# Kernel optimization log

Measured on AMD Instinct MI355X. Metric: run time of the kernel, lower is better.

## Reference

```python
import jax, jax.numpy as jnp
import numpy as np

N = 50000      # nodes
E = 500000     # edges (includes N self-loops)
DIN = 512
DOUT = 256
NEG_SLOPE = 0.01  # torch nn.LeakyReLU default


def setup_inputs() -> dict:
    key = jax.random.key(0)
    k1, k2, k3, k4, k5 = jax.random.split(key, 5)
    x = jax.random.normal(k1, (N, DIN), dtype=jnp.float32)
    # xavier_normal_ with gain=1.414
    std_W = 1.414 * np.sqrt(2.0 / (DIN + DOUT))
    W = jax.random.normal(k2, (DIN, DOUT), dtype=jnp.float32) * std_W
    std_a = 1.414 * np.sqrt(2.0 / (1 + 2 * DOUT))
    a = jax.random.normal(k3, (2 * DOUT,), dtype=jnp.float32) * std_a
    # first N edges are self-loops so every row-sum is nonzero
    loops = jnp.arange(N, dtype=jnp.int32)
    edge_src = jnp.concatenate([loops, jax.random.randint(k4, (E - N,), 0, N, dtype=jnp.int32)])
    edge_dst = jnp.concatenate([loops, jax.random.randint(k5, (E - N,), 0, N, dtype=jnp.int32)])
    return {"x": x, "W": W, "a": a, "edge_src": edge_src, "edge_dst": edge_dst}


def reference(x, W, a, edge_src, edge_dst):
    n = x.shape[0]
    d = W.shape[1]
    h = x @ W  # [N, DOUT]
    # a . [h_src ; h_dst] decomposed per-node, then gathered per-edge
    s_src = h @ a[:d]   # [N]
    s_dst = h @ a[d:]   # [N]
    score = s_src[edge_src] + s_dst[edge_dst]          # [E]
    e = jnp.exp(-jax.nn.leaky_relu(score, NEG_SLOPE))  # [E]
    # sparse softmax denominator: spmm(edge, e, ones) == segment sum over src
    e_rowsum = jax.ops.segment_sum(e, edge_src, num_segments=n)            # [N]
    # numerator: spmm(edge, e, h) == sum_j e_ij * h_j per row i
    h_prime = jax.ops.segment_sum(e[:, None] * h[edge_dst], edge_src, num_segments=n)  # [N, DOUT]
    h_prime = h_prime / e_rowsum[:, None]
    return jax.nn.elu(h_prime)  # concat=True branch
```

## Files before the change

### kernel.cpp

```cpp
#include <hip/hip_runtime.h>
#include <math.h>

#define DIN 512
#define DOUT 256
#define NEG_SLOPE 0.01f

typedef __attribute__((ext_vector_type(8))) short bf16x8;
typedef __attribute__((ext_vector_type(4))) float f32x4;
typedef __attribute__((ext_vector_type(4))) unsigned int u32x4;

__device__ __forceinline__ unsigned short f2bf(float f) {
    unsigned int u = __float_as_uint(f);
    unsigned int r = (u + 0x7FFFu + ((u >> 16) & 1u)) >> 16;
    return (unsigned short)r;
}
__device__ __forceinline__ float bf2f(unsigned short u) {
    return __uint_as_float(((unsigned int)u) << 16);
}
__device__ __forceinline__ unsigned int cvtpk(float lo, float hi) {
    unsigned int r;
    asm("v_cvt_pk_bf16_f32 %0, %1, %2" : "=v"(r) : "v"(lo), "v"(hi));
    return r;
}
__device__ __forceinline__ void gload16(const void* g, void* l) {
    __builtin_amdgcn_global_load_lds(
        (const __attribute__((address_space(1))) void*)g,
        (__attribute__((address_space(3))) void*)l, 16, 0, 0);
}

__global__ void prep(const float* __restrict__ W, unsigned short* __restrict__ Bp,
                     int* __restrict__ deg, float* __restrict__ s_src,
                     float* __restrict__ s_dst, int N) {
    int t = blockIdx.x * blockDim.x + threadIdx.x;
    if (t < (DIN / 32) * (DOUT / 16) * 64) {
        int lane = t & 63;
        int cg = (t >> 6) & 15;
        int ks = t >> 10;
        int l15 = lane & 15, g = lane >> 4;
        int col = cg * 16 + l15;
        int k0 = ks * 32 + g * 8;
        ushort4 lo, hi;
        lo.x = f2bf(W[(size_t)(k0 + 0) * DOUT + col]);
        lo.y = f2bf(W[(size_t)(k0 + 1) * DOUT + col]);
        lo.z = f2bf(W[(size_t)(k0 + 2) * DOUT + col]);
        lo.w = f2bf(W[(size_t)(k0 + 3) * DOUT + col]);
        hi.x = f2bf(W[(size_t)(k0 + 4) * DOUT + col]);
        hi.y = f2bf(W[(size_t)(k0 + 5) * DOUT + col]);
        hi.z = f2bf(W[(size_t)(k0 + 6) * DOUT + col]);
        hi.w = f2bf(W[(size_t)(k0 + 7) * DOUT + col]);
        *(ushort4*)(Bp + (size_t)t * 8) = lo;
        *(ushort4*)(Bp + (size_t)t * 8 + 4) = hi;
    }
    if (t < N) { deg[t] = 0; s_src[t] = 0.f; s_dst[t] = 0.f; }
}

__global__ __launch_bounds__(64, 3) void gemm_k(const float* __restrict__ x,
                                                const unsigned short* __restrict__ Bp,
                                                unsigned short* __restrict__ hb,
                                                const float* __restrict__ av,
                                                float* __restrict__ s_src,
                                                float* __restrict__ s_dst, int M) {
    __shared__ unsigned char As[8192];
    const int lane = threadIdx.x;
    const int l15 = lane & 15;
    const int g = lane >> 4;
    const int m0 = blockIdx.x * 32;
    const int half = blockIdx.y;

    auto stage = [&](int bb, int ks) {
#pragma unroll
        for (int it = 0; it < 4; ++it) {
            int s = it * 64 + lane;
            int row = s >> 3;
            int slot = s & 7;
            int q = slot ^ (row & 7);
            int rg = min(m0 + row, M - 1);
            const float* src = x + (size_t)rg * DIN + ks * 32 + q * 4;
            gload16(src, As + bb * 4096 + it * 1024);
        }
    };

    const unsigned short* pB = Bp + ((size_t)(half * 8) * 64 + lane) * 8;
    f32x4 acc[2][8] = {};

    stage(0, 0);
#pragma unroll
    for (int ks = 0; ks < 16; ++ks) {
        const int bb = ks & 1;
        if (ks < 15) {
            stage(bb ^ 1, ks + 1);
            asm volatile("s_waitcnt vmcnt(4)" ::: "memory");
        } else {
            asm volatile("s_waitcnt vmcnt(0)" ::: "memory");
        }
        const unsigned char* Ab = As + bb * 4096;
        const int rr0 = l15, rr1 = l15 + 16;
        f32x4 v0 = *(const f32x4*)(Ab + rr0 * 128 + (((2 * g) ^ (rr0 & 7)) << 4));
        f32x4 v1 = *(const f32x4*)(Ab + rr0 * 128 + (((2 * g + 1) ^ (rr0 & 7)) << 4));
        f32x4 w0 = *(const f32x4*)(Ab + rr1 * 128 + (((2 * g) ^ (rr1 & 7)) << 4));
        f32x4 w1 = *(const f32x4*)(Ab + rr1 * 128 + (((2 * g + 1) ^ (rr1 & 7)) << 4));
        u32x4 p;
        p.x = cvtpk(v0.x, v0.y); p.y = cvtpk(v0.z, v0.w);
        p.z = cvtpk(v1.x, v1.y); p.w = cvtpk(v1.z, v1.w);
        bf16x8 af0 = *(bf16x8*)&p;
        u32x4 q;
        q.x = cvtpk(w0.x, w0.y); q.y = cvtpk(w0.z, w0.w);
        q.z = cvtpk(w1.x, w1.y); q.w = cvtpk(w1.z, w1.w);
        bf16x8 af1 = *(bf16x8*)&q;
        const unsigned short* pBks = pB + (size_t)ks * 16 * 512;
#pragma unroll
        for (int cg = 0; cg < 8; ++cg) {
            bf16x8 bfr = *(const bf16x8*)(pBks + (size_t)cg * 512);
            acc[0][cg] = __builtin_amdgcn_mfma_f32_16x16x32_bf16(af0, bfr, acc[0][cg], 0, 0, 0);
            acc[1][cg] = __builtin_amdgcn_mfma_f32_16x16x32_bf16(af1, bfr, acc[1][cg], 0, 0, 0);
        }
    }

    float as_[8], ad_[8];
#pragma unroll
    for (int cg = 0; cg < 8; ++cg) {
        int col = half * 128 + cg * 16 + l15;
        as_[cg] = av[col];
        ad_[cg] = av[DOUT + col];
    }
#pragma unroll
    for (int rf = 0; rf < 2; ++rf) {
#pragma unroll
        for (int j = 0; j < 4; ++j) {
            int row = m0 + rf * 16 + g * 4 + j;
            float ps = 0.f, pd = 0.f;
#pragma unroll
            for (int cg = 0; cg < 8; ++cg) {
                float v = acc[rf][cg][j];
                ps += v * as_[cg];
                pd += v * ad_[cg];
            }
#pragma unroll
            for (int off = 1; off < 16; off <<= 1) {
                ps += __shfl_xor(ps, off);
                pd += __shfl_xor(pd, off);
            }
            if (row < M) {
#pragma unroll
                for (int cg = 0; cg < 8; ++cg)
                    hb[(size_t)row * DOUT + half * 128 + cg * 16 + l15] = f2bf(acc[rf][cg][j]);
                if (l15 == 0) {
                    atomicAdd(&s_src[row], ps);
                    atomicAdd(&s_dst[row], pd);
                }
            }
        }
    }
}

__global__ void hist_k(const int* __restrict__ src, int* __restrict__ deg, int E) {
    int i = blockIdx.x * blockDim.x + threadIdx.x;
    if (i < E) atomicAdd(&deg[src[i]], 1);
}

__global__ __launch_bounds__(256) void block_sum(const int* __restrict__ deg, int* __restrict__ bsum, int N) {
    __shared__ int wsum[4];
    int b = blockIdx.x, t = threadIdx.x;
    int idx = b * 1024 + t * 4;
    int s = 0;
    if (idx + 3 < N) {
        int4 v = *(const int4*)(deg + idx);
        s = v.x + v.y + v.z + v.w;
    } else {
        for (int i = 0; i < 4; i++) if (idx + i < N) s += deg[idx + i];
    }
#pragma unroll
    for (int off = 32; off > 0; off >>= 1) s += __shfl_xor(s, off);
    if ((t & 63) == 0) wsum[t >> 6] = s;
    __syncthreads();
    if (t == 0) bsum[b] = wsum[0] + wsum[1] + wsum[2] + wsum[3];
}

__global__ void scan_tops(const int* __restrict__ bsum, int* __restrict__ boff,
                          int* __restrict__ rowptr, int nb, int N, int E) {
    int t = threadIdx.x;
    int v = (t < nb) ? bsum[t] : 0;
    int x = v;
#pragma unroll
    for (int off = 1; off < 64; off <<= 1) {
        int y = __shfl_up(x, off);
        if (t >= off) x += y;
    }
    if (t < nb) boff[t] = x - v;
    if (t == 0) rowptr[N] = E;
}

__global__ __launch_bounds__(256) void scan_blk(const int* __restrict__ deg, const int* __restrict__ boff,
                                                int* __restrict__ rowptr, int* __restrict__ cursor, int N) {
    __shared__ int wsum[4];
    int b = blockIdx.x, t = threadIdx.x;
    int idx = b * 1024 + t * 4;
    int v0 = 0, v1 = 0, v2 = 0, v3 = 0;
    if (idx + 3 < N) {
        int4 v = *(const int4*)(deg + idx);
        v0 = v.x; v1 = v.y; v2 = v.z; v3 = v.w;
    } else if (idx < N) {
        v0 = deg[idx];
        if (idx + 1 < N) v1 = deg[idx + 1];
        if (idx + 2 < N) v2 = deg[idx + 2];
    }
    int s = v0 + v1 + v2 + v3;
    int lane = t & 63, wid = t >> 6;
    int x = s;
#pragma unroll
    for (int off = 1; off < 64; off <<= 1) {
        int y = __shfl_up(x, off);
        if (lane >= off) x += y;
    }
    if (lane == 63) wsum[wid] = x;
    __syncthreads();
    int add = boff[b];
    for (int ww = 0; ww < wid; ++ww) add += wsum[ww];
    int e0 = add + x - s;
    int e1 = e0 + v0, e2 = e1 + v1, e3 = e2 + v2;
    if (idx < N)     { rowptr[idx] = e0;     cursor[idx] = e0; }
    if (idx + 1 < N) { rowptr[idx + 1] = e1; cursor[idx + 1] = e1; }
    if (idx + 2 < N) { rowptr[idx + 2] = e2; cursor[idx + 2] = e2; }
    if (idx + 3 < N) { rowptr[idx + 3] = e3; cursor[idx + 3] = e3; }
}

__global__ void edge_k(const int* __restrict__ src, const int* __restrict__ dst,
                       const float* __restrict__ s_src, const float* __restrict__ s_dst,
                       int* __restrict__ cursor, int2* __restrict__ csr, int E) {
    int i = blockIdx.x * blockDim.x + threadIdx.x;
    if (i >= E) return;
    int s = src[i], d = dst[i];
    float sc = s_src[s] + s_dst[d];
    float lrv = sc > 0.f ? sc : NEG_SLOPE * sc;
    float ev = __expf(-lrv);
    int pos = atomicAdd(&cursor[s], 1);
    csr[pos] = make_int2(d, __float_as_int(ev));
}

__global__ __launch_bounds__(256) void gather_k(const unsigned short* __restrict__ hb,
                                                const int* __restrict__ rowptr,
                                                const int2* __restrict__ csr,
                                                float* __restrict__ out, int N) {
    int gt = blockIdx.x * blockDim.x + threadIdx.x;
    int w = gt >> 6;
    int lane = threadIdx.x & 63;
    if (w >= N) return;
    int s0 = rowptr[w], s1 = rowptr[w + 1];
    float a0 = 0.f, a1 = 0.f, a2 = 0.f, a3 = 0.f, rs = 0.f;
    for (int base = s0; base < s1; base += 64) {
        int cnt = min(64, s1 - base);
        int dv = 0; float ev = 0.f;
        if (lane < cnt) {
            int2 p = csr[base + lane];
            dv = p.x; ev = __int_as_float(p.y);
        }
        int jj = 0;
        for (; jj + 4 <= cnt; jj += 4) {
            int d0 = __shfl(dv, jj), d1 = __shfl(dv, jj + 1), d2 = __shfl(dv, jj + 2), d3 = __shfl(dv, jj + 3);
            float e0 = __shfl(ev, jj), e1 = __shfl(ev, jj + 1), e2 = __shfl(ev, jj + 2), e3 = __shfl(ev, jj + 3);
            ushort4 h0 = *(const ushort4*)(hb + (size_t)d0 * DOUT + lane * 4);
            ushort4 h1 = *(const ushort4*)(hb + (size_t)d1 * DOUT + lane * 4);
            ushort4 h2 = *(const ushort4*)(hb + (size_t)d2 * DOUT + lane * 4);
            ushort4 h3 = *(const ushort4*)(hb + (size_t)d3 * DOUT + lane * 4);
            a0 += e0 * bf2f(h0.x) + e1 * bf2f(h1.x) + e2 * bf2f(h2.x) + e3 * bf2f(h3.x);
            a1 += e0 * bf2f(h0.y) + e1 * bf2f(h1.y) + e2 * bf2f(h2.y) + e3 * bf2f(h3.y);
            a2 += e0 * bf2f(h0.z) + e1 * bf2f(h1.z) + e2 * bf2f(h2.z) + e3 * bf2f(h3.z);
            a3 += e0 * bf2f(h0.w) + e1 * bf2f(h1.w) + e2 * bf2f(h2.w) + e3 * bf2f(h3.w);
            rs += e0 + e1 + e2 + e3;
        }
        for (; jj < cnt; ++jj) {
            int d0 = __shfl(dv, jj);
            float e0 = __shfl(ev, jj);
            ushort4 h0 = *(const ushort4*)(hb + (size_t)d0 * DOUT + lane * 4);
            a0 += e0 * bf2f(h0.x);
            a1 += e0 * bf2f(h0.y);
            a2 += e0 * bf2f(h0.z);
            a3 += e0 * bf2f(h0.w);
            rs += e0;
        }
    }
    float inv = 1.f / rs;
    float4 v;
    v.x = a0 * inv; v.y = a1 * inv; v.z = a2 * inv; v.w = a3 * inv;
    v.x = v.x > 0.f ? v.x : __expf(v.x) - 1.f;
    v.y = v.y > 0.f ? v.y : __expf(v.y) - 1.f;
    v.z = v.z > 0.f ? v.z : __expf(v.z) - 1.f;
    v.w = v.w > 0.f ? v.w : __expf(v.w) - 1.f;
    *(float4*)(out + (size_t)w * DOUT + lane * 4) = v;
}

extern "C" void kernel_launch(void* const* d_in, const int* in_sizes, int n_in,
                              void* d_out, int out_size, void* d_ws, size_t ws_size,
                              hipStream_t stream) {
    const float* x = (const float*)d_in[0];
    const float* W = (const float*)d_in[1];
    const float* a = (const float*)d_in[2];
    const int* edge_src = (const int*)d_in[3];
    const int* edge_dst = (const int*)d_in[4];

    const int N = in_sizes[0] / DIN;
    const int E = in_sizes[3];
    const int nb = (N + 1023) / 1024;

    char* ws = (char*)d_ws;
    size_t off = 0;
    auto alloc = [&](size_t bytes) {
        void* p = ws + off;
        off += (bytes + 15) & ~(size_t)15;
        return p;
    };
    unsigned short* hb = (unsigned short*)alloc((size_t)N * DOUT * 2);
    unsigned short* Bp = (unsigned short*)alloc((size_t)DIN * DOUT * 2);
    int* rowptr = (int*)alloc((size_t)(N + 1) * 4);
    int* deg = (int*)alloc((size_t)N * 4);
    int* cursor = (int*)alloc((size_t)N * 4);
    float* s_src = (float*)alloc((size_t)N * 4);
    float* s_dst = (float*)alloc((size_t)N * 4);
    int2* csr = (int2*)alloc((size_t)E * 8);
    int* bsum = (int*)alloc((size_t)nb * 4);
    int* boff = (int*)alloc((size_t)nb * 4);
    (void)ws_size;

    float* out = (float*)d_out;

    prep<<<(N + 255) / 256, 256, 0, stream>>>(W, Bp, deg, s_src, s_dst, N);
    hist_k<<<(E + 255) / 256, 256, 0, stream>>>(edge_src, deg, E);
    dim3 ggrid((N + 31) / 32, 2);
    gemm_k<<<ggrid, 64, 0, stream>>>(x, Bp, hb, a, s_src, s_dst, N);
    block_sum<<<nb, 256, 0, stream>>>(deg, bsum, N);
    scan_tops<<<1, 64, 0, stream>>>(bsum, boff, rowptr, nb, N, E);
    scan_blk<<<nb, 256, 0, stream>>>(deg, boff, rowptr, cursor, N);
    edge_k<<<(E + 255) / 256, 256, 0, stream>>>(edge_src, edge_dst, s_src, s_dst,
                                                cursor, csr, E);
    gather_k<<<(N + 3) / 4, 256, 0, stream>>>(hb, rowptr, csr, out, N);
}
```

Baseline: 147.3 us.

## Deepen GEMM prefetch pipeline, vectorize histogram, fuse scan-top into block scan

The GEMM now runs a 4-stage LDS ring for x tiles, prefetched two k-steps ahead, and double-buffers the B fragments in registers one step ahead, with explicit vmcnt waits between sched barriers. The goal is to hide global load latency behind the MFMA work. The histogram kernel now reads four source indices per thread with an int4 load. The separate single-block scan_tops launch is removed: each scan_blk block reduces the preceding block sums itself, saving one launch. The costs are more LDS per block and more live registers, which could lower occupancy, and the hand-counted vmcnt values must match the actual number of outstanding loads.

New measurement: 143.5 us. -2.6%, faster.

```diff
diff --git a/kernel.cpp b/kernel.cpp
--- a/kernel.cpp
+++ b/kernel.cpp
@@ -60,7 +60,7 @@
                                                 const float* __restrict__ av,
                                                 float* __restrict__ s_src,
                                                 float* __restrict__ s_dst, int M) {
-    __shared__ unsigned char As[8192];
+    __shared__ unsigned char As[16384];
     const int lane = threadIdx.x;
     const int l15 = lane & 15;
     const int g = lane >> 4;
@@ -82,18 +82,29 @@
 
     const unsigned short* pB = Bp + ((size_t)(half * 8) * 64 + lane) * 8;
     f32x4 acc[2][8] = {};
+    bf16x8 bB[2][8];
 
     stage(0, 0);
+    stage(1, 1);
+#pragma unroll
+    for (int cg = 0; cg < 8; ++cg)
+        bB[0][cg] = *(const bf16x8*)(pB + (size_t)cg * 512);
+
 #pragma unroll
     for (int ks = 0; ks < 16; ++ks) {
-        const int bb = ks & 1;
+        if (ks < 14) stage((ks + 2) & 3, ks + 2);
         if (ks < 15) {
-            stage(bb ^ 1, ks + 1);
-            asm volatile("s_waitcnt vmcnt(4)" ::: "memory");
-        } else {
-            asm volatile("s_waitcnt vmcnt(0)" ::: "memory");
-        }
-        const unsigned char* Ab = As + bb * 4096;
+            const unsigned short* pBn = pB + (size_t)(ks + 1) * 16 * 512;
+#pragma unroll
+            for (int cg = 0; cg < 8; ++cg)
+                bB[(ks + 1) & 1][cg] = *(const bf16x8*)(pBn + (size_t)cg * 512);
+        }
+        __builtin_amdgcn_sched_barrier(0);
+        if (ks < 14)      asm volatile("s_waitcnt vmcnt(24)");
+        else if (ks == 14) asm volatile("s_waitcnt vmcnt(20)");
+        else               asm volatile("s_waitcnt vmcnt(16)");
+        __builtin_amdgcn_sched_barrier(0);
+        const unsigned char* Ab = As + (ks & 3) * 4096;
         const int rr0 = l15, rr1 = l15 + 16;
         f32x4 v0 = *(const f32x4*)(Ab + rr0 * 128 + (((2 * g) ^ (rr0 & 7)) << 4));
         f32x4 v1 = *(const f32x4*)(Ab + rr0 * 128 + (((2 * g + 1) ^ (rr0 & 7)) << 4));
@@ -107,12 +118,10 @@
         q.x = cvtpk(w0.x, w0.y); q.y = cvtpk(w0.z, w0.w);
         q.z = cvtpk(w1.x, w1.y); q.w = cvtpk(w1.z, w1.w);
         bf16x8 af1 = *(bf16x8*)&q;
-        const unsigned short* pBks = pB + (size_t)ks * 16 * 512;
 #pragma unroll
         for (int cg = 0; cg < 8; ++cg) {
-            bf16x8 bfr = *(const bf16x8*)(pBks + (size_t)cg * 512);
-            acc[0][cg] = __builtin_amdgcn_mfma_f32_16x16x32_bf16(af0, bfr, acc[0][cg], 0, 0, 0);
-            acc[1][cg] = __builtin_amdgcn_mfma_f32_16x16x32_bf16(af1, bfr, acc[1][cg], 0, 0, 0);
+            acc[0][cg] = __builtin_amdgcn_mfma_f32_16x16x32_bf16(af0, bB[ks & 1][cg], acc[0][cg], 0, 0, 0);
+            acc[1][cg] = __builtin_amdgcn_mfma_f32_16x16x32_bf16(af1, bB[ks & 1][cg], acc[1][cg], 0, 0, 0);
         }
     }
 
@@ -154,8 +163,16 @@
 }
 
 __global__ void hist_k(const int* __restrict__ src, int* __restrict__ deg, int E) {
-    int i = blockIdx.x * blockDim.x + threadIdx.x;
-    if (i < E) atomicAdd(&deg[src[i]], 1);
+    int i = (blockIdx.x * blockDim.x + threadIdx.x) * 4;
+    if (i + 3 < E) {
+        int4 v = *(const int4*)(src + i);
+        atomicAdd(&deg[v.x], 1);
+        atomicAdd(&deg[v.y], 1);
+        atomicAdd(&deg[v.z], 1);
+        atomicAdd(&deg[v.w], 1);
+    } else {
+        for (int j = i; j < E; ++j) atomicAdd(&deg[src[j]], 1);
+    }
 }
 
 __global__ __launch_bounds__(256) void block_sum(const int* __restrict__ deg, int* __restrict__ bsum, int N) {
@@ -176,24 +193,19 @@
     if (t == 0) bsum[b] = wsum[0] + wsum[1] + wsum[2] + wsum[3];
 }
 
-__global__ void scan_tops(const int* __restrict__ bsum, int* __restrict__ boff,
-                          int* __restrict__ rowptr, int nb, int N, int E) {
-    int t = threadIdx.x;
-    int v = (t < nb) ? bsum[t] : 0;
-    int x = v;
-#pragma unroll
-    for (int off = 1; off < 64; off <<= 1) {
-        int y = __shfl_up(x, off);
-        if (t >= off) x += y;
-    }
-    if (t < nb) boff[t] = x - v;
-    if (t == 0) rowptr[N] = E;
-}
-
-__global__ __launch_bounds__(256) void scan_blk(const int* __restrict__ deg, const int* __restrict__ boff,
-                                                int* __restrict__ rowptr, int* __restrict__ cursor, int N) {
+__global__ __launch_bounds__(256) void scan_blk(const int* __restrict__ deg, const int* __restrict__ bsum,
+                                                int* __restrict__ rowptr, int* __restrict__ cursor,
+                                                int N, int nb, int E) {
     __shared__ int wsum[4];
+    __shared__ int boff_s;
     int b = blockIdx.x, t = threadIdx.x;
+    if (t < 64) {
+        int v = (t < b && t < nb) ? bsum[t] : 0;
+#pragma unroll
+        for (int off = 32; off > 0; off >>= 1) v += __shfl_xor(v, off);
+        if (t == 0) boff_s = v;
+    }
+    if (b == 0 && t == 0) rowptr[N] = E;
     int idx = b * 1024 + t * 4;
     int v0 = 0, v1 = 0, v2 = 0, v3 = 0;
     if (idx + 3 < N) {
@@ -214,7 +226,7 @@
     }
     if (lane == 63) wsum[wid] = x;
     __syncthreads();
-    int add = boff[b];
+    int add = boff_s;
     for (int ww = 0; ww < wid; ++ww) add += wsum[ww];
     int e0 = add + x - s;
     int e1 = e0 + v0, e2 = e1 + v1, e3 = e2 + v2;
@@ -318,18 +330,16 @@
     float* s_dst = (float*)alloc((size_t)N * 4);
     int2* csr = (int2*)alloc((size_t)E * 8);
     int* bsum = (int*)alloc((size_t)nb * 4);
-    int* boff = (int*)alloc((size_t)nb * 4);
     (void)ws_size;
 
     float* out = (float*)d_out;
 
     prep<<<(N + 255) / 256, 256, 0, stream>>>(W, Bp, deg, s_src, s_dst, N);
-    hist_k<<<(E + 255) / 256, 256, 0, stream>>>(edge_src, deg, E);
+    hist_k<<<(E / 4 + 255) / 256, 256, 0, stream>>>(edge_src, deg, E);
     dim3 ggrid((N + 31) / 32, 2);
     gemm_k<<<ggrid, 64, 0, stream>>>(x, Bp, hb, a, s_src, s_dst, N);
     block_sum<<<nb, 256, 0, stream>>>(deg, bsum, N);
-    scan_tops<<<1, 64, 0, stream>>>(bsum, boff, rowptr, nb, N, E);
-    scan_blk<<<nb, 256, 0, stream>>>(deg, boff, rowptr, cursor, N);
+    scan_blk<<<nb, 256, 0, stream>>>(deg, bsum, rowptr, cursor, N, nb, E);
     edge_k<<<(E + 255) / 256, 256, 0, stream>>>(edge_src, edge_dst, s_src, s_dst,
                                                 cursor, csr, E);
     gather_k<<<(N + 3) / 4, 256, 0, stream>>>(hb, rowptr, csr, out, N);
```
